# Kernel tuning notes

Measured on AMD Instinct MI355X. Metric: run time of the kernel, lower is better.

The kernel has to match this reference:

```python
import jax, jax.numpy as jnp
import numpy as np

N = 8192
IN_DIM = 256
OUT_DIM = 128
ALPHA = 0.2  # LeakyReLU negative slope
MASK_VAL = -9e15


def setup_inputs() -> dict:
    key = jax.random.key(0)
    k1, k2, k3, k4 = jax.random.split(key, 4)
    adjacency = jax.random.randint(k1, (N, N), 0, 2, dtype=jnp.int32)
    X = jax.random.normal(k2, (N, IN_DIM), dtype=jnp.float32)
    # kaiming-normal-ish scale
    W = jax.random.normal(k3, (IN_DIM, OUT_DIM), dtype=jnp.float32) * np.sqrt(2.0 / IN_DIM)
    a = jax.random.normal(k4, (2 * OUT_DIM, 1), dtype=jnp.float32) * np.sqrt(2.0 / (2 * OUT_DIM))
    return {"adjacency": adjacency, "X": X, "W": W, "a": a}


def reference(adjacency, X, W, a):
    Wh = X @ W  # [N, D]
    # e[i,j] = lrelu([Wh_i ; Wh_j] @ a) = lrelu(Wh@a1 + (Wh@a2)^T)
    a1 = a[:OUT_DIM, 0]   # [D]
    a2 = a[OUT_DIM:, 0]   # [D]
    e = (Wh @ a1)[:, None] + (Wh @ a2)[None, :]  # [N, N]
    e = jax.nn.leaky_relu(e, negative_slope=ALPHA)
    scores = jnp.where(adjacency > 0, e, jnp.asarray(MASK_VAL, e.dtype))
    attention = jax.nn.softmax(scores, axis=1)  # dropout p=0 -> identity
    h_prime = attention @ Wh  # [N, D]
    return jax.nn.elu(h_prime)
```

## Files before the change

kernel.cpp:

```cpp
#include <hip/hip_runtime.h>
#include <hip/hip_bf16.h>

#define NN 8192
#define KDIM 256
#define DDIM 128

typedef __attribute__((ext_vector_type(8))) short short8;
typedef __attribute__((ext_vector_type(4))) float floatx4;
typedef __attribute__((ext_vector_type(4))) int intx4;

__device__ __forceinline__ unsigned short f2bf(float x) {
    unsigned int u = __float_as_uint(x);
    return (unsigned short)((u + 0x8000u) >> 16);
}

__global__ void k_trip(float* out, float v) {
    if (threadIdx.x == 0 && blockIdx.x == 0) out[0] = v;
}

__global__ void kA_swizzleW(const float* __restrict__ W, unsigned short* __restrict__ WB) {
    int gid = blockIdx.x * blockDim.x + threadIdx.x;
    int kt = gid >> 9, nt = (gid >> 6) & 7, lane = gid & 63;
    int quad = lane >> 4, c = lane & 15;
    short8 pack;
#pragma unroll
    for (int t = 0; t < 8; ++t)
        pack[t] = (short)f2bf(W[(kt * 32 + quad * 8 + t) * DDIM + nt * 16 + c]);
    *(short8*)(WB + ((size_t)(kt * 8 + nt) * 64 + lane) * 8) = pack;
}

__global__ __launch_bounds__(256) void kB_wh(
        const float* __restrict__ X,
        const unsigned short* __restrict__ WB,
        const float* __restrict__ a,
        unsigned short* __restrict__ WhB,
        float* __restrict__ f, float* __restrict__ g) {
    __shared__ unsigned short tile[64 * 128];
    int tid = threadIdx.x;
    int wave = tid >> 6, lane = tid & 63;
    int quad = lane >> 4, c = lane & 15;
    int rowbase = blockIdx.x * 64 + wave * 16;

    floatx4 acc[8];
#pragma unroll
    for (int nt = 0; nt < 8; ++nt) acc[nt] = (floatx4)(0.0f);

    const short8* WB8 = (const short8*)WB;
#pragma unroll
    for (int ks = 0; ks < 8; ++ks) {
        const float* xp = X + (size_t)(rowbase + c) * KDIM + ks * 32 + quad * 8;
        floatx4 x0 = *(const floatx4*)xp;
        floatx4 x1 = *(const floatx4*)(xp + 4);
        short8 afrag;
#pragma unroll
        for (int t = 0; t < 4; ++t) { afrag[t] = (short)f2bf(x0[t]); afrag[4 + t] = (short)f2bf(x1[t]); }
#pragma unroll
        for (int nt = 0; nt < 8; ++nt) {
            short8 b = WB8[(ks * 8 + nt) * 64 + lane];
            acc[nt] = __builtin_amdgcn_mfma_f32_16x16x32_bf16(afrag, b, acc[nt], 0, 0, 0);
        }
    }

    float fp[4] = {0.f, 0.f, 0.f, 0.f}, gp[4] = {0.f, 0.f, 0.f, 0.f};
#pragma unroll
    for (int nt = 0; nt < 8; ++nt) {
        float a1 = a[nt * 16 + c];
        float a2 = a[DDIM + nt * 16 + c];
#pragma unroll
        for (int r = 0; r < 4; ++r) {
            fp[r] += acc[nt][r] * a1;
            gp[r] += acc[nt][r] * a2;
        }
    }
#pragma unroll
    for (int m = 1; m < 16; m <<= 1) {
#pragma unroll
        for (int r = 0; r < 4; ++r) {
            fp[r] += __shfl_xor(fp[r], m);
            gp[r] += __shfl_xor(gp[r], m);
        }
    }
    if (c == 0) {
#pragma unroll
        for (int r = 0; r < 4; ++r) {
            f[rowbase + quad * 4 + r] = fp[r];
            g[rowbase + quad * 4 + r] = gp[r];
        }
    }

#pragma unroll
    for (int nt = 0; nt < 8; ++nt)
#pragma unroll
        for (int r = 0; r < 4; ++r)
            tile[(wave * 16 + quad * 4 + r) * 128 + nt * 16 + c] = f2bf(acc[nt][r]);
    __syncthreads();

    int kt2 = wave >> 1;
#pragma unroll
    for (int ntj = 0; ntj < 4; ++ntj) {
        int nt = (wave & 1) * 4 + ntj;
        short8 pack;
#pragma unroll
        for (int t = 0; t < 8; ++t)
            pack[t] = (short)tile[(kt2 * 32 + quad * 8 + t) * 128 + nt * 16 + c];
        *(short8*)(WhB + ((size_t)((blockIdx.x * 2 + kt2) * 8 + nt) * 64 + lane) * 8) = pack;
    }
}

__global__ __launch_bounds__(256, 3) void kC_attn(
        const int* __restrict__ adj,
        const unsigned short* __restrict__ WhB,
        const float* __restrict__ f, const float* __restrict__ g,
        float* __restrict__ out) {
    __shared__ float smem[8192];
    int tid = threadIdx.x;
    int wave = tid >> 6, lane = tid & 63;
    int quad = lane >> 4, c = lane & 15;
    int rowbase = blockIdx.x * 16;

    for (int i = tid; i < NN / 4; i += 256)
        ((floatx4*)smem)[i] = ((const floatx4*)g)[i];
    __syncthreads();

    float f0 = f[rowbase + c];

    floatx4 acc[8];
#pragma unroll
    for (int nt = 0; nt < 8; ++nt) acc[nt] = (floatx4)(0.0f);
    float l0 = 0.0f;

    const intx4* arow = (const intx4*)(adj + (size_t)(rowbase + c) * NN);
    const short8* WhB8 = (const short8*)WhB;

    intx4 A0a = arow[(0 * 4 + wave) * 8 + quad * 2], A0b = arow[(0 * 4 + wave) * 8 + quad * 2 + 1];
    intx4 A1a = arow[(1 * 4 + wave) * 8 + quad * 2], A1b = arow[(1 * 4 + wave) * 8 + quad * 2 + 1];

    for (int it = 0; it < 64; ++it) {
        int j4n = (((it + 2) & 63) * 4 + wave) * 8 + quad * 2;
        intx4 A2a = arow[j4n], A2b = arow[j4n + 1];

        int J32 = it * 4 + wave;
        short8 bfr[8];
#pragma unroll
        for (int nt = 0; nt < 8; ++nt)
            bfr[nt] = WhB8[((size_t)J32 * 8 + nt) * 64 + lane];

        int gb = J32 * 32 + quad * 8;
        floatx4 g0 = *(const floatx4*)&smem[gb];
        floatx4 g1 = *(const floatx4*)&smem[gb + 4];

        short8 afr;
#pragma unroll
        for (int u = 0; u < 4; ++u) {
            float x, E;
            x = f0 + g0[u]; x = fmaxf(x, 0.2f * x);
            E = (A0a[u] > 0) ? __expf(x) : 0.0f; l0 += E; afr[u] = (short)f2bf(E);
            x = f0 + g1[u]; x = fmaxf(x, 0.2f * x);
            E = (A0b[u] > 0) ? __expf(x) : 0.0f; l0 += E; afr[4 + u] = (short)f2bf(E);
        }

#pragma unroll
        for (int nt = 0; nt < 8; ++nt)
            acc[nt] = __builtin_amdgcn_mfma_f32_16x16x32_bf16(afr, bfr[nt], acc[nt], 0, 0, 0);

        A0a = A1a; A0b = A1b; A1a = A2a; A1b = A2b;
    }

    __syncthreads();
    smem[7000 + wave * 64 + lane] = l0;
    __syncthreads();
    if (tid < 16) {
        float s = 0.0f;
#pragma unroll
        for (int w = 0; w < 4; ++w)
#pragma unroll
            for (int q = 0; q < 4; ++q)
                s += smem[7000 + w * 64 + q * 16 + tid];
        smem[7256 + tid] = (s > 0.0f) ? 1.0f / s : 0.0f;
    }
    __syncthreads();

    if (wave >= 2) {
        float* b = &smem[(wave - 2) * 2304 + lane * 36];
#pragma unroll
        for (int nt = 0; nt < 8; ++nt) *(floatx4*)&b[nt * 4] = acc[nt];
    }
    __syncthreads();
    if (wave < 2) {
        float* b = &smem[wave * 2304 + lane * 36];
#pragma unroll
        for (int nt = 0; nt < 8; ++nt) acc[nt] += *(const floatx4*)&b[nt * 4];
    }
    __syncthreads();
    if (wave == 1) {
        float* b = &smem[lane * 36];
#pragma unroll
        for (int nt = 0; nt < 8; ++nt) *(floatx4*)&b[nt * 4] = acc[nt];
    }
    __syncthreads();

    if (wave == 0) {
        float* b = &smem[lane * 36];
#pragma unroll
        for (int nt = 0; nt < 8; ++nt) acc[nt] += *(const floatx4*)&b[nt * 4];
        float linv[4];
#pragma unroll
        for (int r = 0; r < 4; ++r) linv[r] = smem[7256 + quad * 4 + r];
#pragma unroll
        for (int nt = 0; nt < 8; ++nt)
#pragma unroll
            for (int r = 0; r < 4; ++r) {
                float h = acc[nt][r] * linv[r];
                h = (h > 0.0f) ? h : expm1f(h);
                out[(size_t)(rowbase + quad * 4 + r) * DDIM + nt * 16 + c] = h;
            }
    }
}

extern "C" void kernel_launch(void* const* d_in, const int* in_sizes, int n_in,
                              void* d_out, int out_size, void* d_ws, size_t ws_size,
                              hipStream_t stream) {
    float* out = (float*)d_out;

    const void *p_adj = nullptr, *p_X = nullptr, *p_W = nullptr, *p_a = nullptr;
    for (int i = 0; i < n_in; ++i) {
        switch (in_sizes[i]) {
            case NN * NN:     p_adj = d_in[i]; break;
            case NN * KDIM:   p_X   = d_in[i]; break;
            case KDIM * DDIM: p_W   = d_in[i]; break;
            case 2 * DDIM:    p_a   = d_in[i]; break;
            default: break;
        }
    }
    if (!p_adj || !p_X || !p_W || !p_a) {
        k_trip<<<dim3(1), dim3(64), 0, stream>>>(out, 99999.0f);
        return;
    }

    size_t off_WB  = 0;
    size_t off_WhB = off_WB + 65536;
    size_t off_f   = off_WhB + (size_t)NN * DDIM * 2;
    size_t off_g   = off_f + NN * 4;
    size_t needed  = off_g + NN * 4;
    if (ws_size < needed) {
        k_trip<<<dim3(1), dim3(64), 0, stream>>>(out, 12345.0f);
        return;
    }
    char* ws = (char*)d_ws;
    unsigned short* WB  = (unsigned short*)(ws + off_WB);
    unsigned short* WhB = (unsigned short*)(ws + off_WhB);
    float*          f   = (float*)(ws + off_f);
    float*          g   = (float*)(ws + off_g);

    const int*   adj = (const int*)p_adj;
    const float* X   = (const float*)p_X;
    const float* W   = (const float*)p_W;
    const float* a   = (const float*)p_a;

    kA_swizzleW<<<dim3(16), dim3(256), 0, stream>>>(W, WB);
    kB_wh<<<dim3(128), dim3(256), 0, stream>>>(X, WB, a, WhB, f, g);
    kC_attn<<<dim3(512), dim3(256), 0, stream>>>(adj, WhB, f, g, out);
}
```

Before: 413.4 us.

## Bitpack adjacency into a mask and process 32 rows per attention block

Adds a pre-pass that compresses the int32 adjacency matrix into a bit mask with wave ballots. The attention kernel then stages each block's mask rows in shared memory and handles 32 rows per block with 8 waves, so each Wh fragment load is reused for two MFMA row tiles. The partial sums from the 8 waves are combined with a tree reduction in shared memory. The full 256 MB adjacency read still happens in the pre-pass, so the aim is mainly to halve Wh traffic and give the main kernel a more regular load pattern, at the cost of an extra kernel launch, more shared memory and lower occupancy.

```diff
diff --git a/kernel.cpp b/kernel.cpp
--- a/kernel.cpp
+++ b/kernel.cpp
@@ -16,6 +16,26 @@
 
 __global__ void k_trip(float* out, float v) {
     if (threadIdx.x == 0 && blockIdx.x == 0) out[0] = v;
+}
+
+__global__ __launch_bounds__(256) void kP_bitpack(const int* __restrict__ adj,
+                                                  unsigned long long* __restrict__ mask) {
+    int wid  = (blockIdx.x * 256 + threadIdx.x) >> 6;
+    int lane = threadIdx.x & 63;
+    const int* base = adj + (size_t)wid * 16384;
+    unsigned long long* mbase = mask + (size_t)wid * 256;
+    for (int s = 0; s < 256; s += 8) {
+        int v[8];
+#pragma unroll
+        for (int u = 0; u < 8; ++u) v[u] = base[(s + u) * 64 + lane];
+        unsigned long long b[8];
+#pragma unroll
+        for (int u = 0; u < 8; ++u) b[u] = __ballot(v[u] > 0);
+        if (lane == 0) {
+#pragma unroll
+            for (int u = 0; u < 8; ++u) mbase[s + u] = b[u];
+        }
+    }
 }
 
 __global__ void kA_swizzleW(const float* __restrict__ W, unsigned short* __restrict__ WB) {
@@ -107,39 +127,43 @@
     }
 }
 
-__global__ __launch_bounds__(256, 3) void kC_attn(
-        const int* __restrict__ adj,
+__global__ __launch_bounds__(512) void kC_attn(
+        const unsigned long long* __restrict__ mask,
         const unsigned short* __restrict__ WhB,
         const float* __restrict__ f, const float* __restrict__ g,
         float* __restrict__ out) {
-    __shared__ float smem[8192];
+    __shared__ float smem[16384];
+    __shared__ __align__(16) unsigned char msk[32 * 1040];
     int tid = threadIdx.x;
     int wave = tid >> 6, lane = tid & 63;
     int quad = lane >> 4, c = lane & 15;
-    int rowbase = blockIdx.x * 16;
-
-    for (int i = tid; i < NN / 4; i += 256)
+    int rowbase = blockIdx.x * 32;
+
+    for (int i = tid; i < NN / 4; i += 512)
         ((floatx4*)smem)[i] = ((const floatx4*)g)[i];
+    {
+        const floatx4* msrc = (const floatx4*)(mask + (size_t)rowbase * 128);
+#pragma unroll
+        for (int p = 0; p < 4; ++p) {
+            int idx = p * 512 + tid;
+            int r = idx >> 6, ch = idx & 63;
+            *(floatx4*)&msk[r * 1040 + ch * 16] = msrc[idx];
+        }
+    }
     __syncthreads();
 
     float f0 = f[rowbase + c];
-
-    floatx4 acc[8];
-#pragma unroll
-    for (int nt = 0; nt < 8; ++nt) acc[nt] = (floatx4)(0.0f);
-    float l0 = 0.0f;
-
-    const intx4* arow = (const intx4*)(adj + (size_t)(rowbase + c) * NN);
+    float f1 = f[rowbase + 16 + c];
+
+    floatx4 acc0[8], acc1[8];
+#pragma unroll
+    for (int nt = 0; nt < 8; ++nt) { acc0[nt] = (floatx4)(0.0f); acc1[nt] = (floatx4)(0.0f); }
+    float l0 = 0.0f, l1 = 0.0f;
+
     const short8* WhB8 = (const short8*)WhB;
 
-    intx4 A0a = arow[(0 * 4 + wave) * 8 + quad * 2], A0b = arow[(0 * 4 + wave) * 8 + quad * 2 + 1];
-    intx4 A1a = arow[(1 * 4 + wave) * 8 + quad * 2], A1b = arow[(1 * 4 + wave) * 8 + quad * 2 + 1];
-
-    for (int it = 0; it < 64; ++it) {
-        int j4n = (((it + 2) & 63) * 4 + wave) * 8 + quad * 2;
-        intx4 A2a = arow[j4n], A2b = arow[j4n + 1];
-
-        int J32 = it * 4 + wave;
+    for (int t = 0; t < 32; ++t) {
+        int J32 = t * 8 + wave;
         short8 bfr[8];
 #pragma unroll
         for (int nt = 0; nt < 8; ++nt)
@@ -149,71 +173,85 @@
         floatx4 g0 = *(const floatx4*)&smem[gb];
         floatx4 g1 = *(const floatx4*)&smem[gb + 4];
 
-        short8 afr;
+        unsigned int mb0 = msk[c * 1040 + J32 * 4 + quad];
+        unsigned int mb1 = msk[(c + 16) * 1040 + J32 * 4 + quad];
+
+        short8 afr0, afr1;
 #pragma unroll
         for (int u = 0; u < 4; ++u) {
             float x, E;
             x = f0 + g0[u]; x = fmaxf(x, 0.2f * x);
-            E = (A0a[u] > 0) ? __expf(x) : 0.0f; l0 += E; afr[u] = (short)f2bf(E);
+            E = (mb0 & (1u << u)) ? __expf(x) : 0.0f; l0 += E; afr0[u] = (short)f2bf(E);
             x = f0 + g1[u]; x = fmaxf(x, 0.2f * x);
-            E = (A0b[u] > 0) ? __expf(x) : 0.0f; l0 += E; afr[4 + u] = (short)f2bf(E);
-        }
-
-#pragma unroll
-        for (int nt = 0; nt < 8; ++nt)
-            acc[nt] = __builtin_amdgcn_mfma_f32_16x16x32_bf16(afr, bfr[nt], acc[nt], 0, 0, 0);
-
-        A0a = A1a; A0b = A1b; A1a = A2a; A1b = A2b;
-    }
-
-    __syncthreads();
-    smem[7000 + wave * 64 + lane] = l0;
-    __syncthreads();
-    if (tid < 16) {
+            E = (mb0 & (1u << (4 + u))) ? __expf(x) : 0.0f; l0 += E; afr0[4 + u] = (short)f2bf(E);
+            x = f1 + g0[u]; x = fmaxf(x, 0.2f * x);
+            E = (mb1 & (1u << u)) ? __expf(x) : 0.0f; l1 += E; afr1[u] = (short)f2bf(E);
+            x = f1 + g1[u]; x = fmaxf(x, 0.2f * x);
+            E = (mb1 & (1u << (4 + u))) ? __expf(x) : 0.0f; l1 += E; afr1[4 + u] = (short)f2bf(E);
+        }
+
+#pragma unroll
+        for (int nt = 0; nt < 8; ++nt) {
+            acc0[nt] = __builtin_amdgcn_mfma_f32_16x16x32_bf16(afr0, bfr[nt], acc0[nt], 0, 0, 0);
+            acc1[nt] = __builtin_amdgcn_mfma_f32_16x16x32_bf16(afr1, bfr[nt], acc1[nt], 0, 0, 0);
+        }
+    }
+
+    __syncthreads();
+    smem[wave * 128 + lane] = l0;
+    smem[wave * 128 + 64 + lane] = l1;
+    __syncthreads();
+    if (tid < 32) {
+        int mt = tid >> 4, cc = tid & 15;
         float s = 0.0f;
 #pragma unroll
-        for (int w = 0; w < 4; ++w)
+        for (int w = 0; w < 8; ++w)
 #pragma unroll
             for (int q = 0; q < 4; ++q)
-                s += smem[7000 + w * 64 + q * 16 + tid];
-        smem[7256 + tid] = (s > 0.0f) ? 1.0f / s : 0.0f;
-    }
-    __syncthreads();
-
-    if (wave >= 2) {
-        float* b = &smem[(wave - 2) * 2304 + lane * 36];
-#pragma unroll
-        for (int nt = 0; nt < 8; ++nt) *(floatx4*)&b[nt * 4] = acc[nt];
-    }
-    __syncthreads();
-    if (wave < 2) {
-        float* b = &smem[wave * 2304 + lane * 36];
-#pragma unroll
-        for (int nt = 0; nt < 8; ++nt) acc[nt] += *(const floatx4*)&b[nt * 4];
-    }
-    __syncthreads();
-    if (wave == 1) {
-        float* b = &smem[lane * 36];
-#pragma unroll
-        for (int nt = 0; nt < 8; ++nt) *(floatx4*)&b[nt * 4] = acc[nt];
-    }
-    __syncthreads();
-
+                s += smem[w * 128 + mt * 64 + q * 16 + cc];
+        smem[1024 + tid] = s;
+    }
+    __syncthreads();
+    float linv0[4], linv1[4];
     if (wave == 0) {
-        float* b = &smem[lane * 36];
-#pragma unroll
-        for (int nt = 0; nt < 8; ++nt) acc[nt] += *(const floatx4*)&b[nt * 4];
-        float linv[4];
-#pragma unroll
-        for (int r = 0; r < 4; ++r) linv[r] = smem[7256 + quad * 4 + r];
-#pragma unroll
-        for (int nt = 0; nt < 8; ++nt)
+#pragma unroll
+        for (int r = 0; r < 4; ++r) {
+            float l0v = smem[1024 + quad * 4 + r];
+            float l1v = smem[1024 + 16 + quad * 4 + r];
+            linv0[r] = (l0v > 0.0f) ? 1.0f / l0v : 0.0f;
+            linv1[r] = (l1v > 0.0f) ? 1.0f / l1v : 0.0f;
+        }
+    }
+    __syncthreads();
+
+    for (int half = 4; half >= 1; half >>= 1) {
+        if (wave >= half && wave < 2 * half) {
+            floatx4* buf = (floatx4*)&smem[(wave - half) * 4096 + lane * 64];
+#pragma unroll
+            for (int nt = 0; nt < 8; ++nt) { buf[nt] = acc0[nt]; buf[8 + nt] = acc1[nt]; }
+        }
+        __syncthreads();
+        if (wave < half) {
+            floatx4* buf = (floatx4*)&smem[wave * 4096 + lane * 64];
+#pragma unroll
+            for (int nt = 0; nt < 8; ++nt) { acc0[nt] += buf[nt]; acc1[nt] += buf[8 + nt]; }
+        }
+        __syncthreads();
+    }
+
+    if (wave == 0) {
+#pragma unroll
+        for (int nt = 0; nt < 8; ++nt) {
 #pragma unroll
             for (int r = 0; r < 4; ++r) {
-                float h = acc[nt][r] * linv[r];
+                float h = acc0[nt][r] * linv0[r];
                 h = (h > 0.0f) ? h : expm1f(h);
                 out[(size_t)(rowbase + quad * 4 + r) * DDIM + nt * 16 + c] = h;
+                float h2 = acc1[nt][r] * linv1[r];
+                h2 = (h2 > 0.0f) ? h2 : expm1f(h2);
+                out[(size_t)(rowbase + 16 + quad * 4 + r) * DDIM + nt * 16 + c] = h2;
             }
+        }
     }
 }
 
@@ -241,7 +279,8 @@
     size_t off_WhB = off_WB + 65536;
     size_t off_f   = off_WhB + (size_t)NN * DDIM * 2;
     size_t off_g   = off_f + NN * 4;
-    size_t needed  = off_g + NN * 4;
+    size_t off_mk  = off_g + NN * 4;
+    size_t needed  = off_mk + (size_t)NN * NN / 8;
     if (ws_size < needed) {
         k_trip<<<dim3(1), dim3(64), 0, stream>>>(out, 12345.0f);
         return;
@@ -251,13 +290,15 @@
     unsigned short* WhB = (unsigned short*)(ws + off_WhB);
     float*          f   = (float*)(ws + off_f);
     float*          g   = (float*)(ws + off_g);
+    unsigned long long* mask = (unsigned long long*)(ws + off_mk);
 
     const int*   adj = (const int*)p_adj;
     const float* X   = (const float*)p_X;
     const float* W   = (const float*)p_W;
     const float* a   = (const float*)p_a;
 
+    kP_bitpack<<<dim3(1024), dim3(256), 0, stream>>>(adj, mask);
     kA_swizzleW<<<dim3(16), dim3(256), 0, stream>>>(W, WB);
     kB_wh<<<dim3(128), dim3(256), 0, stream>>>(X, WB, a, WhB, f, g);
-    kC_attn<<<dim3(512), dim3(256), 0, stream>>>(adj, WhB, f, g, out);
-}
+    kC_attn<<<dim3(256), dim3(512), 0, stream>>>(mask, WhB, f, g, out);
+}
```

New measurement: 438.9 us. 1.06x slower.
